# Kernel optimization log

Measured on AMD Instinct MI355X. Metric: run time of the kernel, lower is better.

Reference implementation:

```python
import jax, jax.numpy as jnp
import numpy as np

N = 8192
IN_FEATURES = 512
OUT_FEATURES = 256
ALPHA = 0.2  # LeakyReLU negative slope
MASK_VAL = -1e11


def setup_inputs() -> dict:
    key = jax.random.key(0)
    k_h, k_adj, k_w, k_a1, k_a2 = jax.random.split(key, 5)
    h = jax.random.normal(k_h, (N, IN_FEATURES), dtype=jnp.float32)
    adj = jax.random.randint(k_adj, (N, N), 0, 2, dtype=jnp.int32)
    # xavier_uniform with gain=1.414 for Linear weight [out, in]
    def xavier(k, fan_out, fan_in, gain=1.414):
        bound = gain * np.sqrt(6.0 / (fan_in + fan_out))
        return jax.random.uniform(k, (fan_out, fan_in), dtype=jnp.float32,
                                  minval=-bound, maxval=bound)
    W = xavier(k_w, OUT_FEATURES, IN_FEATURES)          # linear_w.weight
    a1 = xavier(k_a1, 1, OUT_FEATURES)[0]               # linear_a_1.weight -> [out]
    a2 = xavier(k_a2, 1, OUT_FEATURES)[0]               # linear_a_2.weight -> [out]
    return {"h": h, "W": W, "a1": a1, "a2": a2, "adj": adj}


def reference(h, W, a1, a2, adj):
    # wh: [N, F_out]
    wh = jnp.einsum("ni,oi->no", h, W)
    wh1 = wh @ a1  # [N]
    wh2 = wh @ a2  # [N]
    # additive attention scores e_ij = leakyrelu(wh1_i + wh2_j): [N, N]
    e = jax.nn.leaky_relu(wh1[:, None] + wh2[None, :], negative_slope=ALPHA)
    scores = jnp.where(adj > 0, e, MASK_VAL)
    attention = jax.nn.softmax(scores, axis=-1)  # dropout p=0 -> identity
    h_new = attention @ wh  # [N, F_out]
    return jax.nn.elu(h_new)  # concat=True path
```

## Files before the change

### kernel.cpp

```cpp
#include <hip/hip_runtime.h>


typedef __attribute__((ext_vector_type(8))) short short8;
typedef __attribute__((ext_vector_type(4))) float f32x4;

#define LOG2E 1.4426950408889634f

__device__ __forceinline__ unsigned short f2bf(float f) {
  unsigned int u = __float_as_uint(f);
  unsigned int r = u + 0x7FFFu + ((u >> 16) & 1u);
  return (unsigned short)(r >> 16);
}

__global__ __launch_bounds__(512) void k_u(const float* __restrict__ W,
                                           const float* __restrict__ a1,
                                           const float* __restrict__ a2,
                                           float* __restrict__ u1,
                                           float* __restrict__ u2) {
  __shared__ float p1[16][32], p2[16][32];
  const int tid = threadIdx.x;
  const int kk = tid & 31, og = tid >> 5;
  const int k0 = blockIdx.x * 32;
  float s1 = 0.f, s2 = 0.f;
#pragma unroll
  for (int j = 0; j < 16; j++) {
    const int o = og * 16 + j;
    const float w = W[(size_t)o * 512 + k0 + kk];
    s1 += w * a1[o];
    s2 += w * a2[o];
  }
  p1[og][kk] = s1;
  p2[og][kk] = s2;
  __syncthreads();
  if (tid < 32) {
    float t1 = 0.f, t2 = 0.f;
#pragma unroll
    for (int g = 0; g < 16; g++) { t1 += p1[g][tid]; t2 += p2[g][tid]; }
    u1[k0 + tid] = t1;
    u2[k0 + tid] = t2;
  }
}

__global__ __launch_bounds__(256) void k_rowvec(const float* __restrict__ h,
                                                const float* __restrict__ u1,
                                                const float* __restrict__ u2,
                                                float* __restrict__ wh1,
                                                float* __restrict__ wh2,
                                                float* __restrict__ pmax) {
  __shared__ float su1[512], su2[512];
  __shared__ float smax[4];
  const int tid = threadIdx.x;
  for (int i = tid; i < 512; i += 256) { su1[i] = u1[i]; su2[i] = u2[i]; }
  __syncthreads();
  const int lane = tid & 63;
  const int row = blockIdx.x * 4 + (tid >> 6);
  const float* hp = h + (size_t)row * 512 + lane * 8;
  float4 x0 = *(const float4*)hp;
  float4 x1 = *(const float4*)(hp + 4);
  const float* q1 = su1 + lane * 8;
  const float* q2 = su2 + lane * 8;
  float s1 = x0.x * q1[0] + x0.y * q1[1] + x0.z * q1[2] + x0.w * q1[3]
           + x1.x * q1[4] + x1.y * q1[5] + x1.z * q1[6] + x1.w * q1[7];
  float s2 = x0.x * q2[0] + x0.y * q2[1] + x0.z * q2[2] + x0.w * q2[3]
           + x1.x * q2[4] + x1.y * q2[5] + x1.z * q2[6] + x1.w * q2[7];
#pragma unroll
  for (int off = 32; off >= 1; off >>= 1) {
    s1 += __shfl_xor(s1, off);
    s2 += __shfl_xor(s2, off);
  }
  if (lane == 0) {
    wh1[row] = s1 * LOG2E;
    wh2[row] = s2 * LOG2E;
    smax[tid >> 6] = s2 * LOG2E;
  }
  __syncthreads();
  if (tid == 0)
    pmax[blockIdx.x] = fmaxf(fmaxf(smax[0], smax[1]), fmaxf(smax[2], smax[3]));
}

__global__ __launch_bounds__(512, 1) void k_wh(const float* __restrict__ h,
                                               const float* __restrict__ W,
                                               unsigned short* __restrict__ whT,
                                               const float* __restrict__ pmax,
                                               float* __restrict__ gmax) {
  __shared__ uint4 lds[2560];
  __shared__ float sred[8];
  const int tid = threadIdx.x;
  if (blockIdx.x == 0) {
    float m = -3.0e38f;
    for (int i = tid; i < 2048; i += 512) m = fmaxf(m, pmax[i]);
#pragma unroll
    for (int off = 32; off >= 1; off >>= 1) m = fmaxf(m, __shfl_xor(m, off));
    if ((tid & 63) == 0) sred[tid >> 6] = m;
    __syncthreads();
    if (tid == 0) {
      float g = sred[0];
#pragma unroll
      for (int i = 1; i < 8; i++) g = fmaxf(g, sred[i]);
      gmax[0] = g;
    }
  }
  const int i0 = blockIdx.x * 64;
  const int lane = tid & 63, wid = tid >> 6;
  const int wm = wid >> 2, wn = wid & 3;
  const int l16 = lane & 15, lq = lane >> 4;
  const int hr = tid >> 3, hc = tid & 7;
  const int wr = tid >> 1, wc = tid & 1;

  f32x4 acc[2][4] = {};

  for (int t = 0; t < 8; t++) {
    const int k0 = t * 64;
    const float* hp = h + (size_t)(i0 + hr) * 512 + k0 + hc * 8;
    float4 hx = *(const float4*)hp;
    float4 hy = *(const float4*)(hp + 4);
    const float* wp = W + (size_t)wr * 512 + k0 + wc * 32;
    float4 wv[8];
#pragma unroll
    for (int q = 0; q < 8; q++) wv[q] = *(const float4*)(wp + q * 4);

    __syncthreads();
    uint4 hw;
    hw.x = (unsigned)f2bf(hx.x) | ((unsigned)f2bf(hx.y) << 16);
    hw.y = (unsigned)f2bf(hx.z) | ((unsigned)f2bf(hx.w) << 16);
    hw.z = (unsigned)f2bf(hy.x) | ((unsigned)f2bf(hy.y) << 16);
    hw.w = (unsigned)f2bf(hy.z) | ((unsigned)f2bf(hy.w) << 16);
    lds[hr * 8 + (hc ^ (hr & 7))] = hw;
#pragma unroll
    for (int q = 0; q < 4; q++) {
      uint4 ww;
      ww.x = (unsigned)f2bf(wv[2 * q].x) | ((unsigned)f2bf(wv[2 * q].y) << 16);
      ww.y = (unsigned)f2bf(wv[2 * q].z) | ((unsigned)f2bf(wv[2 * q].w) << 16);
      ww.z = (unsigned)f2bf(wv[2 * q + 1].x) | ((unsigned)f2bf(wv[2 * q + 1].y) << 16);
      ww.w = (unsigned)f2bf(wv[2 * q + 1].z) | ((unsigned)f2bf(wv[2 * q + 1].w) << 16);
      lds[512 + wr * 8 + ((wc * 4 + q) ^ (wr & 7))] = ww;
    }
    __syncthreads();
#pragma unroll
    for (int ks = 0; ks < 2; ks++) {
      const int r0 = wm * 32 + l16, r1 = r0 + 16;
      short8 fa0 = *(const short8*)&lds[r0 * 8 + ((ks * 4 + lq) ^ (r0 & 7))];
      short8 fa1 = *(const short8*)&lds[r1 * 8 + ((ks * 4 + lq) ^ (r1 & 7))];
#pragma unroll
      for (int fn = 0; fn < 4; fn++) {
        const int bn = wn * 64 + fn * 16 + l16;
        short8 fb = *(const short8*)&lds[512 + bn * 8 + ((ks * 4 + lq) ^ (bn & 7))];
        acc[0][fn] = __builtin_amdgcn_mfma_f32_16x16x32_bf16(fa0, fb, acc[0][fn], 0, 0, 0);
        acc[1][fn] = __builtin_amdgcn_mfma_f32_16x16x32_bf16(fa1, fb, acc[1][fn], 0, 0, 0);
      }
    }
  }
#pragma unroll
  for (int fm = 0; fm < 2; fm++) {
#pragma unroll
    for (int fn = 0; fn < 4; fn++) {
      const int n = wn * 64 + fn * 16 + l16;
      const int m0 = i0 + wm * 32 + fm * 16 + lq * 4;
      uint2 o;
      o.x = (unsigned)f2bf(acc[fm][fn][0]) | ((unsigned)f2bf(acc[fm][fn][1]) << 16);
      o.y = (unsigned)f2bf(acc[fm][fn][2]) | ((unsigned)f2bf(acc[fm][fn][3]) << 16);
      *(uint2*)(whT + (size_t)n * 8192 + m0) = o;
    }
  }
}

struct PFR {
  int4 l0, l1, l2, l3, h0, h1, h2, h3;
};

__global__ __launch_bounds__(512, 1) void k_attn(
    const int* __restrict__ adj, const unsigned short* __restrict__ whT,
    const float* __restrict__ wh1v, const float* __restrict__ wh2v,
    const float* __restrict__ gmax,
    float* __restrict__ out0, float* __restrict__ out1,
    float* __restrict__ out2, float* __restrict__ out3,
    float* __restrict__ denp) {
  __shared__ uint4 ring[2][2048];
  __shared__ float wh2s[2048];
  const int NT = 32;
  const int tid = threadIdx.x;
  const int bid = blockIdx.x;
  const int sb = (bid & 7) >> 1;
  const int mb = ((bid >> 3) << 1) | (bid & 1);
  const int i0 = mb * 128;
  const int jbase = sb * 2048;
  const int lane = tid & 63, wid = tid >> 6;
  const int wm = wid >> 1, wn = wid & 1;
  const int l16 = lane & 15, q = lane >> 4;
  const int row_lo = i0 + wm * 32 + l16;

  if (tid < 512) ((float4*)wh2s)[tid] = ((const float4*)(wh2v + jbase))[tid];

  const float M2 = gmax[0];
  const float w1lo = wh1v[row_lo];
  const float w1hi = wh1v[row_lo + 16];
  float tv = w1lo + M2;
  const float Milo = tv > 0.f ? tv : 0.2f * tv;
  tv = w1hi + M2;
  const float Mihi = tv > 0.f ? tv : 0.2f * tv;
  const float c1lo = w1lo - Milo, c2lo = 0.2f * w1lo - Milo;
  const float c1hi = w1hi - Mihi, c2hi = 0.2f * w1hi - Mihi;

  const int* ap_lo = adj + (size_t)row_lo * 8192 + jbase + q * 8;
  const int* ap_hi = ap_lo + 16 * 8192;

  f32x4 accL[8] = {}, accH[8] = {};
  float dsL = 0.f, dsH = 0.f;
  short8 paL0, paL1, paH0, paH1;
  PFR PA, PB;

#define PFLOAD(R, T)                              \
  do {                                            \
    const int o_ = (((T) < NT) ? (T) : 0) * 64;   \
    R.l0 = *(const int4*)(ap_lo + o_);            \
    R.l1 = *(const int4*)(ap_lo + o_ + 4);        \
    R.l2 = *(const int4*)(ap_lo + o_ + 32);       \
    R.l3 = *(const int4*)(ap_lo + o_ + 36);       \
    R.h0 = *(const int4*)(ap_hi + o_);            \
    R.h1 = *(const int4*)(ap_hi + o_ + 4);        \
    R.h2 = *(const int4*)(ap_hi + o_ + 32);       \
    R.h3 = *(const int4*)(ap_hi + o_ + 36);       \
  } while (0)

#define COMPUTE(R, T)                                                          \
  do {                                                                         \
    const int o_ = (((T) < NT) ? (T) : 0) * 64 + q * 8;                        \
    float4 z0 = *(const float4*)(wh2s + o_);                                   \
    float4 z1 = *(const float4*)(wh2s + o_ + 4);                               \
    float4 z2 = *(const float4*)(wh2s + o_ + 32);                              \
    float4 z3 = *(const float4*)(wh2s + o_ + 36);                              \
    float zv[16] = {z0.x, z0.y, z0.z, z0.w, z1.x, z1.y, z1.z, z1.w,            \
                    z2.x, z2.y, z2.z, z2.w, z3.x, z3.y, z3.z, z3.w};           \
    int al[16] = {R.l0.x, R.l0.y, R.l0.z, R.l0.w, R.l1.x, R.l1.y, R.l1.z,      \
                  R.l1.w, R.l2.x, R.l2.y, R.l2.z, R.l2.w, R.l3.x, R.l3.y,      \
                  R.l3.z, R.l3.w};                                             \
    int ah[16] = {R.h0.x, R.h0.y, R.h0.z, R.h0.w, R.h1.x, R.h1.y, R.h1.z,      \
                  R.h1.w, R.h2.x, R.h2.y, R.h2.z, R.h2.w, R.h3.x, R.h3.y,      \
                  R.h3.z, R.h3.w};                                             \
    float pl[16], ph[16];                                                      \
    _Pragma("unroll") for (int i = 0; i < 16; i++) {                           \
      float e1 = fmaxf(c1lo + zv[i], __builtin_fmaf(0.2f, zv[i], c2lo));       \
      float p = (al[i] > 0) ? __builtin_amdgcn_exp2f(e1) : 0.f;                \
      pl[i] = p;                                                               \
      dsL += p;                                                                \
      float e2 = fmaxf(c1hi + zv[i], __builtin_fmaf(0.2f, zv[i], c2hi));       \
      p = (ah[i] > 0) ? __builtin_amdgcn_exp2f(e2) : 0.f;                      \
      ph[i] = p;                                                               \
      dsH += p;                                                                \
    }                                                                          \
    _Pragma("unroll") for (int i = 0; i < 8; i++) {                            \
      paL0[i] = (short)f2bf(pl[i]);                                            \
      paL1[i] = (short)f2bf(pl[8 + i]);                                        \
      paH0[i] = (short)f2bf(ph[i]);                                            \
      paH1[i] = (short)f2bf(ph[8 + i]);                                        \
    }                                                                          \
  } while (0)

#define STAGE(TT, SLOT)                                                        \
  do {                                                                         \
    const int tt_ = ((TT) < NT) ? (TT) : 0;                                    \
    const size_t gj_ = (size_t)(jbase + tt_ * 64);                             \
    _Pragma("unroll") for (int kq = 0; kq < 4; kq++) {                         \
      const int L = kq * 512 + tid;                                            \
      const int row = L >> 3, sub = L & 7;                                     \
      const int boff = (sub * 16) ^ ((row & 7) << 4);                          \
      const char* src_ = (const char*)(whT + (size_t)row * 8192 + gj_) + boff; \
      char* dst_ = (char*)ring[SLOT] + L * 16;                                 \
      __builtin_amdgcn_global_load_lds(                                        \
          (const __attribute__((address_space(1))) unsigned int*)src_,         \
          (__attribute__((address_space(3))) unsigned int*)dst_, 16, 0, 0);    \
    }                                                                          \
  } while (0)

#define FENCE asm volatile("s_waitcnt vmcnt(8)" ::: "memory")

#define MFMAPH(SLOT)                                                           \
  do {                                                                         \
    const char* lb_ = (const char*)ring[SLOT];                                 \
    _Pragma("unroll") for (int nb = 0; nb < 8; nb++) {                         \
      const int n_ = wn * 128 + nb * 16 + l16;                                 \
      const int rb_ = n_ * 128;                                                \
      const int sw_ = (n_ & 7) << 4;                                           \
      short8 fb0 = *(const short8*)(lb_ + rb_ + ((q * 16) ^ sw_));             \
      short8 fb1 = *(const short8*)(lb_ + rb_ + ((64 + q * 16) ^ sw_));        \
      accL[nb] = __builtin_amdgcn_mfma_f32_16x16x32_bf16(paL0, fb0, accL[nb], 0, 0, 0); \
      accL[nb] = __builtin_amdgcn_mfma_f32_16x16x32_bf16(paL1, fb1, accL[nb], 0, 0, 0); \
      accH[nb] = __builtin_amdgcn_mfma_f32_16x16x32_bf16(paH0, fb0, accH[nb], 0, 0, 0); \
      accH[nb] = __builtin_amdgcn_mfma_f32_16x16x32_bf16(paH1, fb1, accH[nb], 0, 0, 0); \
    }                                                                          \
  } while (0)

  PFLOAD(PA, 0);
  STAGE(0, 0);
  __syncthreads();

  for (int t = 0; t < NT; t += 2) {
    PFLOAD(PB, t + 1);
    COMPUTE(PA, t);
    FENCE;
    __builtin_amdgcn_s_barrier();
    STAGE(t + 1, 1);
    MFMAPH(0);
    PFLOAD(PA, t + 2);
    COMPUTE(PB, t + 1);
    FENCE;
    __builtin_amdgcn_s_barrier();
    STAGE(t + 2, 0);
    MFMAPH(1);
  }

#undef PFLOAD
#undef COMPUTE
#undef STAGE
#undef FENCE
#undef MFMAPH

  float* outp = (sb == 0) ? out0 : (sb == 1) ? out1 : (sb == 2) ? out2 : out3;
  const int r0 = i0 + wm * 32 + q * 4;
#pragma unroll
  for (int nb = 0; nb < 8; nb++) {
    const int col = wn * 128 + nb * 16 + l16;
#pragma unroll
    for (int r = 0; r < 4; r++) {
      outp[(size_t)(r0 + r) * 256 + col] = accL[nb][r];
      outp[(size_t)(r0 + 16 + r) * 256 + col] = accH[nb][r];
    }
  }

  dsL += __shfl_xor(dsL, 16);
  dsL += __shfl_xor(dsL, 32);
  dsH += __shfl_xor(dsH, 16);
  dsH += __shfl_xor(dsH, 32);
  if (wn == 0 && lane < 16) {
    denp[sb * 8192 + i0 + wm * 32 + lane] = dsL;
    denp[sb * 8192 + i0 + wm * 32 + 16 + lane] = dsH;
  }
}

__global__ __launch_bounds__(256) void k_out(float* __restrict__ out,
                                             const float* __restrict__ p1,
                                             const float* __restrict__ p2,
                                             const float* __restrict__ p3,
                                             const float* __restrict__ denp) {
  const int idx = blockIdx.x * 256 + threadIdx.x;
  const int row = idx >> 6;
  float4 o = ((const float4*)out)[idx];
  float4 a = ((const float4*)p1)[idx];
  float4 b = ((const float4*)p2)[idx];
  float4 c = ((const float4*)p3)[idx];
  const float inv =
      1.0f / (denp[row] + denp[8192 + row] + denp[16384 + row] + denp[24576 + row]);
  float v0 = (o.x + a.x + b.x + c.x) * inv;
  float v1 = (o.y + a.y + b.y + c.y) * inv;
  float v2 = (o.z + a.z + b.z + c.z) * inv;
  float v3 = (o.w + a.w + b.w + c.w) * inv;
  v0 = v0 > 0.f ? v0 : expm1f(v0);
  v1 = v1 > 0.f ? v1 : expm1f(v1);
  v2 = v2 > 0.f ? v2 : expm1f(v2);
  v3 = v3 > 0.f ? v3 : expm1f(v3);
  ((float4*)out)[idx] = make_float4(v0, v1, v2, v3);
}

extern "C" void kernel_launch(void* const* d_in, const int* in_sizes, int n_in,
                              void* d_out, int out_size, void* d_ws, size_t ws_size,
                              hipStream_t stream) {
  const float* h = (const float*)d_in[0];
  const float* W = (const float*)d_in[1];
  const float* a1 = (const float*)d_in[2];
  const float* a2 = (const float*)d_in[3];
  const int* adj = (const int*)d_in[4];
  float* out = (float*)d_out;
  char* ws = (char*)d_ws;

  unsigned short* whT = (unsigned short*)ws;
  float* part1 = (float*)(ws + (4u << 20));
  float* part2 = (float*)(ws + (12u << 20));
  float* part3 = (float*)(ws + (20u << 20));
  float* denp = (float*)(ws + (28u << 20));
  float* wh1 = denp + 4 * 8192;
  float* wh2 = wh1 + 8192;
  float* pmax = wh2 + 8192;
  float* u1 = pmax + 2048;
  float* u2 = u1 + 512;
  float* gmax = u2 + 512;

  hipLaunchKernelGGL(k_u, dim3(16), dim3(512), 0, stream, W, a1, a2, u1, u2);
  hipLaunchKernelGGL(k_rowvec, dim3(2048), dim3(256), 0, stream, h, u1, u2, wh1,
                     wh2, pmax);
  hipLaunchKernelGGL(k_wh, dim3(128), dim3(512), 0, stream, h, W, whT, pmax, gmax);
  hipLaunchKernelGGL(k_attn, dim3(256), dim3(512), 0, stream, adj, whT, wh1,
                     wh2, gmax, out, part1, part2, part3, denp);
  hipLaunchKernelGGL(k_out, dim3(2048), dim3(256), 0, stream, out, part1, part2,
                     part3, denp);
  (void)in_sizes; (void)n_in; (void)out_size; (void)ws_size;
}
```

Measured before the change: 153.4 us.

## Pack adjacency into bitmask in a pre-pass for the attention kernel

Adds a k_mask kernel that reads the int32 adjacency matrix once and packs it into 64-bit ballot bitmasks, one word per 64 columns. The attention kernel now prefetches two 64-bit words per tile instead of eight int4 vectors, and tests bits rather than comparing integers. The vmcnt wait threshold is lowered to match the smaller number of outstanding loads. The aim is to cut the attention kernel's register pressure and memory-latency stalls on the adjacency stream. The cost is an extra launch and a full streaming pass over the adjacency matrix plus an 8MB write.

```diff
diff --git a/kernel.cpp b/kernel.cpp
--- a/kernel.cpp
+++ b/kernel.cpp
@@ -10,6 +10,29 @@
   unsigned int u = __float_as_uint(f);
   unsigned int r = u + 0x7FFFu + ((u >> 16) & 1u);
   return (unsigned short)(r >> 16);
+}
+
+__global__ __launch_bounds__(256) void k_mask(const int* __restrict__ adj,
+                                              unsigned long long* __restrict__ bm) {
+  const int row = blockIdx.x * 4 + (threadIdx.x >> 6);
+  const int lane = threadIdx.x & 63;
+  const int* ap = adj + (size_t)row * 8192 + lane;
+  unsigned long long* bp = bm + (size_t)row * 128;
+#pragma unroll 2
+  for (int c = 0; c < 128; c += 4) {
+    int v0 = ap[(c + 0) * 64];
+    int v1 = ap[(c + 1) * 64];
+    int v2 = ap[(c + 2) * 64];
+    int v3 = ap[(c + 3) * 64];
+    unsigned long long m0 = __ballot(v0 > 0);
+    unsigned long long m1 = __ballot(v1 > 0);
+    unsigned long long m2 = __ballot(v2 > 0);
+    unsigned long long m3 = __ballot(v3 > 0);
+    if (lane == 0) {
+      *(ulonglong2*)(bp + c) = make_ulonglong2(m0, m1);
+      *(ulonglong2*)(bp + c + 2) = make_ulonglong2(m2, m3);
+    }
+  }
 }
 
 __global__ __launch_bounds__(512) void k_u(const float* __restrict__ W,
@@ -165,11 +188,11 @@
 }
 
 struct PFR {
-  int4 l0, l1, l2, l3, h0, h1, h2, h3;
+  unsigned long long lo, hi;
 };
 
 __global__ __launch_bounds__(512, 1) void k_attn(
-    const int* __restrict__ adj, const unsigned short* __restrict__ whT,
+    const unsigned long long* __restrict__ bm, const unsigned short* __restrict__ whT,
     const float* __restrict__ wh1v, const float* __restrict__ wh2v,
     const float* __restrict__ gmax,
     float* __restrict__ out0, float* __restrict__ out1,
@@ -201,8 +224,8 @@
   const float c1lo = w1lo - Milo, c2lo = 0.2f * w1lo - Milo;
   const float c1hi = w1hi - Mihi, c2hi = 0.2f * w1hi - Mihi;
 
-  const int* ap_lo = adj + (size_t)row_lo * 8192 + jbase + q * 8;
-  const int* ap_hi = ap_lo + 16 * 8192;
+  const unsigned long long* bmp_lo = bm + (size_t)row_lo * 128 + sb * 32;
+  const unsigned long long* bmp_hi = bmp_lo + 16 * 128;
 
   f32x4 accL[8] = {}, accH[8] = {};
   float dsL = 0.f, dsH = 0.f;
@@ -211,15 +234,9 @@
 
 #define PFLOAD(R, T)                              \
   do {                                            \
-    const int o_ = (((T) < NT) ? (T) : 0) * 64;   \
-    R.l0 = *(const int4*)(ap_lo + o_);            \
-    R.l1 = *(const int4*)(ap_lo + o_ + 4);        \
-    R.l2 = *(const int4*)(ap_lo + o_ + 32);       \
-    R.l3 = *(const int4*)(ap_lo + o_ + 36);       \
-    R.h0 = *(const int4*)(ap_hi + o_);            \
-    R.h1 = *(const int4*)(ap_hi + o_ + 4);        \
-    R.h2 = *(const int4*)(ap_hi + o_ + 32);       \
-    R.h3 = *(const int4*)(ap_hi + o_ + 36);       \
+    const int t_ = ((T) < NT) ? (T) : 0;          \
+    R.lo = bmp_lo[t_];                            \
+    R.hi = bmp_hi[t_];                            \
   } while (0)
 
 #define COMPUTE(R, T)                                                          \
@@ -231,20 +248,19 @@
     float4 z3 = *(const float4*)(wh2s + o_ + 36);                              \
     float zv[16] = {z0.x, z0.y, z0.z, z0.w, z1.x, z1.y, z1.z, z1.w,            \
                     z2.x, z2.y, z2.z, z2.w, z3.x, z3.y, z3.z, z3.w};           \
-    int al[16] = {R.l0.x, R.l0.y, R.l0.z, R.l0.w, R.l1.x, R.l1.y, R.l1.z,      \
-                  R.l1.w, R.l2.x, R.l2.y, R.l2.z, R.l2.w, R.l3.x, R.l3.y,      \
-                  R.l3.z, R.l3.w};                                             \
-    int ah[16] = {R.h0.x, R.h0.y, R.h0.z, R.h0.w, R.h1.x, R.h1.y, R.h1.z,      \
-                  R.h1.w, R.h2.x, R.h2.y, R.h2.z, R.h2.w, R.h3.x, R.h3.y,      \
-                  R.h3.z, R.h3.w};                                             \
+    const unsigned msl[2] = {(unsigned)(R.lo >> (q * 8)),                      \
+                             (unsigned)(R.lo >> (32 + q * 8))};                \
+    const unsigned msh[2] = {(unsigned)(R.hi >> (q * 8)),                      \
+                             (unsigned)(R.hi >> (32 + q * 8))};                \
     float pl[16], ph[16];                                                      \
     _Pragma("unroll") for (int i = 0; i < 16; i++) {                           \
       float e1 = fmaxf(c1lo + zv[i], __builtin_fmaf(0.2f, zv[i], c2lo));       \
-      float p = (al[i] > 0) ? __builtin_amdgcn_exp2f(e1) : 0.f;                \
+      float p = (msl[i >> 3] & (1u << (i & 7))) ? __builtin_amdgcn_exp2f(e1)   \
+                                                : 0.f;                         \
       pl[i] = p;                                                               \
       dsL += p;                                                                \
       float e2 = fmaxf(c1hi + zv[i], __builtin_fmaf(0.2f, zv[i], c2hi));       \
-      p = (ah[i] > 0) ? __builtin_amdgcn_exp2f(e2) : 0.f;                      \
+      p = (msh[i >> 3] & (1u << (i & 7))) ? __builtin_amdgcn_exp2f(e2) : 0.f;  \
       ph[i] = p;                                                               \
       dsH += p;                                                                \
     }                                                                          \
@@ -272,7 +288,7 @@
     }                                                                          \
   } while (0)
 
-#define FENCE asm volatile("s_waitcnt vmcnt(8)" ::: "memory")
+#define FENCE asm volatile("s_waitcnt vmcnt(2)" ::: "memory")
 
 #define MFMAPH(SLOT)                                                           \
   do {                                                                         \
@@ -383,12 +399,14 @@
   float* u1 = pmax + 2048;
   float* u2 = u1 + 512;
   float* gmax = u2 + 512;
-
+  unsigned long long* bm = (unsigned long long*)(ws + (29u << 20));
+
+  hipLaunchKernelGGL(k_mask, dim3(2048), dim3(256), 0, stream, adj, bm);
   hipLaunchKernelGGL(k_u, dim3(16), dim3(512), 0, stream, W, a1, a2, u1, u2);
   hipLaunchKernelGGL(k_rowvec, dim3(2048), dim3(256), 0, stream, h, u1, u2, wh1,
                      wh2, pmax);
   hipLaunchKernelGGL(k_wh, dim3(128), dim3(512), 0, stream, h, W, whT, pmax, gmax);
-  hipLaunchKernelGGL(k_attn, dim3(256), dim3(512), 0, stream, adj, whT, wh1,
+  hipLaunchKernelGGL(k_attn, dim3(256), dim3(512), 0, stream, bm, whT, wh1,
                      wh2, gmax, out, part1, part2, part3, denp);
   hipLaunchKernelGGL(k_out, dim3(2048), dim3(256), 0, stream, out, part1, part2,
                      part3, denp);
```

Result: slower. 176.2 us (+14.8%).
